# Performance work log

Hardware: AMD Instinct MI355X
Metric: run time of the kernel (lower is better)

## Reference

```python
import jax, jax.numpy as jnp
import numpy as np

NUM_QUBITS = 12
BOND_DIM = 8
DIM = 2 ** NUM_QUBITS  # 4096


def setup_inputs() -> dict:
    key = jax.random.key(0)
    k0, k1, k2, k3 = jax.random.split(key, 4)
    core0 = jax.random.normal(k0, (2, BOND_DIM), dtype=jnp.float32) * 0.5
    cores_mid = jax.random.normal(k1, (NUM_QUBITS - 2, BOND_DIM, 2, BOND_DIM), dtype=jnp.float32) * 0.5
    core_last = jax.random.normal(k2, (BOND_DIM, 2), dtype=jnp.float32) * 0.5
    A = jax.random.normal(k3, (DIM, DIM), dtype=jnp.float32)
    H = 0.5 * (A + A.T)  # Hamiltonians are symmetric
    return {"core0": core0, "cores_mid": cores_mid, "core_last": core_last, "H": H}


def _build_state(core0, cores_mid, core_last):
    # Sequential MPS contraction: state grows (2^k, D) site by site.
    state = core0  # (2, D)
    n_mid = cores_mid.shape[0]
    D = core0.shape[1]
    for i in range(n_mid):  # fixed, small layer loop (not a data-dim loop)
        # (S, a) x (a, p, b) -> (S, p, b) -> (S*2, b)
        state = jnp.einsum('sa,apb->spb', state, cores_mid[i]).reshape(-1, D)
    # (S, a) x (a, p) -> flat state vector of length 2^n
    psi = jnp.einsum('sa,ap->sp', state, core_last).reshape(-1)
    return psi


def reference(core0, cores_mid, core_last, H):
    psi = _build_state(core0, cores_mid, core_last)  # (2^n,)
    norm = jnp.dot(psi, psi)
    hpsi = H @ psi
    energy = jnp.dot(psi, hpsi) / norm          # <psi|H|psi>/<psi|psi>
    e2 = jnp.dot(psi, H @ hpsi) / norm          # <psi|H^2|psi>/<psi|psi>
    variance = jnp.maximum(e2 - energy * energy, 0.0)
    return jnp.stack([energy, variance])
```

## Files before the change

kernel.cpp:

```cpp
#include <hip/hip_runtime.h>
#include <hip/hip_bf16.h>


#define DIM 4096
#define BOND 8
#define NMID 10


__global__ __launch_bounds__(256) void build_psi_kernel(
    const float* __restrict__ core0,
    const float* __restrict__ cores_mid,
    const float* __restrict__ core_last,
    float* __restrict__ psi_g,
    double* __restrict__ acc) {
  __shared__ float c0[16];
  __shared__ float cm[NMID * 128];
  __shared__ float cl[16];

  if (threadIdx.x < 16) {
    c0[threadIdx.x] = core0[threadIdx.x];
    cl[threadIdx.x] = core_last[threadIdx.x];
  }
  for (int j = threadIdx.x; j < NMID * 128; j += 256) cm[j] = cores_mid[j];
  __syncthreads();

  const int idx = blockIdx.x * 256 + threadIdx.x;

  float v[BOND], nv[BOND];
  const int s0 = (idx >> 11) & 1;
#pragma unroll
  for (int a = 0; a < BOND; a++) v[a] = c0[s0 * BOND + a];

#pragma unroll
  for (int i = 0; i < NMID; i++) {
    const int p = (idx >> (10 - i)) & 1;
    const float* M = &cm[i * 128 + p * BOND];
#pragma unroll
    for (int b = 0; b < BOND; b++) nv[b] = v[0] * M[b];
#pragma unroll
    for (int a = 1; a < BOND; a++) {
#pragma unroll
      for (int b = 0; b < BOND; b++) nv[b] += v[a] * M[a * 16 + b];
    }
#pragma unroll
    for (int a = 0; a < BOND; a++) v[a] = nv[a];
  }

  const int pl = idx & 1;
  float ps = 0.f;
#pragma unroll
  for (int a = 0; a < BOND; a++) ps += v[a] * cl[a * 2 + pl];

  psi_g[idx] = ps;

  float sq = ps * ps;
#pragma unroll
  for (int off = 32; off > 0; off >>= 1) sq += __shfl_down(sq, off, 64);
  if ((threadIdx.x & 63) == 0) atomicAdd(&acc[0], (double)sq);
}

__global__ __launch_bounds__(256) void matvec_dots_kernel(
    const float* __restrict__ H,
    const float* __restrict__ psi_g,
    double* __restrict__ acc) {
  __shared__ float psi_s[DIM];
  __shared__ float wave_hpsi[4];

#pragma unroll
  for (int k = 0; k < 4; k++) {
    const int j = (k * 256 + threadIdx.x) * 4;
    *reinterpret_cast<float4*>(&psi_s[j]) =
        *reinterpret_cast<const float4*>(&psi_g[j]);
  }
  __syncthreads();

  const int wave = threadIdx.x >> 6;
  const int lane = threadIdx.x & 63;
  const int row = blockIdx.x * 4 + wave;
  const float* __restrict__ Hrow = H + (size_t)row * DIM;

  float sum = 0.f;
#pragma unroll
  for (int it = 0; it < 16; it++) {
    const int j = (it * 64 + lane) * 4;
    const float4 h = *reinterpret_cast<const float4*>(&Hrow[j]);
    const float4 p = *reinterpret_cast<const float4*>(&psi_s[j]);
    sum += h.x * p.x + h.y * p.y + h.z * p.z + h.w * p.w;
  }
#pragma unroll
  for (int off = 32; off > 0; off >>= 1) sum += __shfl_down(sum, off, 64);
  if (lane == 0) wave_hpsi[wave] = sum;
  __syncthreads();

  if (threadIdx.x == 0) {
    double ph = 0.0, hh = 0.0;
#pragma unroll
    for (int w = 0; w < 4; w++) {
      const double hp = (double)wave_hpsi[w];
      const double pr = (double)psi_s[blockIdx.x * 4 + w];
      ph += pr * hp;
      hh += hp * hp;
    }
    atomicAdd(&acc[1], ph);
    atomicAdd(&acc[2], hh);
  }
}

__global__ void finalize_kernel(const double* __restrict__ acc,
                                float* __restrict__ out) {
  const double norm = acc[0];
  const double e = acc[1] / norm;
  const double e2 = acc[2] / norm;
  double var = e2 - e * e;
  if (var < 0.0) var = 0.0;
  out[0] = (float)e;
  out[1] = (float)var;
}

extern "C" void kernel_launch(void* const* d_in, const int* in_sizes, int n_in,
                              void* d_out, int out_size, void* d_ws, size_t ws_size,
                              hipStream_t stream) {
  const float* core0 = (const float*)d_in[0];
  const float* cores_mid = (const float*)d_in[1];
  const float* core_last = (const float*)d_in[2];
  const float* H = (const float*)d_in[3];

  float* psi = (float*)d_ws;
  double* acc = (double*)((char*)d_ws + DIM * sizeof(float));

  hipMemsetAsync(acc, 0, 3 * sizeof(double), stream);
  build_psi_kernel<<<DIM / 256, 256, 0, stream>>>(core0, cores_mid, core_last, psi, acc);
  matvec_dots_kernel<<<DIM / 4, 256, 0, stream>>>(H, psi, acc);
  finalize_kernel<<<1, 1, 0, stream>>>(acc, (float*)d_out);
}
```

Baseline: 128.6 us.

## Exploit symmetry of H to read only upper-triangle tiles in matvec

Replaces the full row-wise matvec with a tiled symmetric matvec: each block handles one upper-triangular 128x128 tile of H and adds contributions to both y_I (via H x_J) and y_J (via H^T x_I). This roughly halves the HBM traffic for the 64 MB H read. Results go to hpsi through float atomics, and a single-block kernel then computes the norm, energy and variance, which removes the memset and finalize launches. In exchange it adds per-row wave shuffle reductions, float atomic contention on hpsi, and a serial loop in each block to decode its tile index.

After: 123.4 us. 4.0% less time.

```diff
diff --git a/kernel.cpp b/kernel.cpp
--- a/kernel.cpp
+++ b/kernel.cpp
@@ -5,6 +5,9 @@
 #define DIM 4096
 #define BOND 8
 #define NMID 10
+#define T 128
+#define NT (DIM / T)
+#define NPAIRS (NT * (NT + 1) / 2)
 
 
 __global__ __launch_bounds__(256) void build_psi_kernel(
@@ -12,7 +15,7 @@
     const float* __restrict__ cores_mid,
     const float* __restrict__ core_last,
     float* __restrict__ psi_g,
-    double* __restrict__ acc) {
+    float* __restrict__ hpsi_g) {
   __shared__ float c0[16];
   __shared__ float cm[NMID * 128];
   __shared__ float cl[16];
@@ -25,6 +28,7 @@
   __syncthreads();
 
   const int idx = blockIdx.x * 256 + threadIdx.x;
+  hpsi_g[idx] = 0.f;
 
   float v[BOND], nv[BOND];
   const int s0 = (idx >> 11) & 1;
@@ -52,69 +56,94 @@
   for (int a = 0; a < BOND; a++) ps += v[a] * cl[a * 2 + pl];
 
   psi_g[idx] = ps;
-
-  float sq = ps * ps;
-#pragma unroll
-  for (int off = 32; off > 0; off >>= 1) sq += __shfl_down(sq, off, 64);
-  if ((threadIdx.x & 63) == 0) atomicAdd(&acc[0], (double)sq);
 }
 
-__global__ __launch_bounds__(256) void matvec_dots_kernel(
+__global__ __launch_bounds__(256) void symv_kernel(
     const float* __restrict__ H,
     const float* __restrict__ psi_g,
-    double* __restrict__ acc) {
-  __shared__ float psi_s[DIM];
-  __shared__ float wave_hpsi[4];
+    float* __restrict__ hpsi_g) {
+  int rem = blockIdx.x;
+  int bi = 0;
+  while (rem >= NT - bi) { rem -= (NT - bi); ++bi; }
+  const int bj = bi + rem;
+  const bool diag = (bi == bj);
 
-#pragma unroll
-  for (int k = 0; k < 4; k++) {
-    const int j = (k * 256 + threadIdx.x) * 4;
-    *reinterpret_cast<float4*>(&psi_s[j]) =
-        *reinterpret_cast<const float4*>(&psi_g[j]);
+  __shared__ float xI[T], xJ[T], yI_s[T], yJp[4 * T];
+
+  if (threadIdx.x < T) {
+    xI[threadIdx.x] = psi_g[bi * T + threadIdx.x];
+    xJ[threadIdx.x] = psi_g[bj * T + threadIdx.x];
   }
   __syncthreads();
 
   const int wave = threadIdx.x >> 6;
   const int lane = threadIdx.x & 63;
-  const int row = blockIdx.x * 4 + wave;
-  const float* __restrict__ Hrow = H + (size_t)row * DIM;
+  const float* __restrict__ base = H + (size_t)(bi * T) * DIM + bj * T;
 
-  float sum = 0.f;
+  float aJx = 0.f, aJy = 0.f;
+  const float pJx = xJ[lane * 2], pJy = xJ[lane * 2 + 1];
+
+#pragma unroll 4
+  for (int k = 0; k < T / 4; ++k) {
+    const int r = k * 4 + wave;
+    const float2 a = *reinterpret_cast<const float2*>(base + (size_t)r * DIM + lane * 2);
+    const float xr = xI[r];
+    aJx += a.x * xr;
+    aJy += a.y * xr;
+    float d = a.x * pJx + a.y * pJy;
 #pragma unroll
-  for (int it = 0; it < 16; it++) {
-    const int j = (it * 64 + lane) * 4;
-    const float4 h = *reinterpret_cast<const float4*>(&Hrow[j]);
-    const float4 p = *reinterpret_cast<const float4*>(&psi_s[j]);
-    sum += h.x * p.x + h.y * p.y + h.z * p.z + h.w * p.w;
+    for (int off = 32; off > 0; off >>= 1) d += __shfl_down(d, off, 64);
+    if (lane == 0) yI_s[r] = d;
   }
-#pragma unroll
-  for (int off = 32; off > 0; off >>= 1) sum += __shfl_down(sum, off, 64);
-  if (lane == 0) wave_hpsi[wave] = sum;
+
+  yJp[wave * T + lane * 2] = aJx;
+  yJp[wave * T + lane * 2 + 1] = aJy;
   __syncthreads();
 
-  if (threadIdx.x == 0) {
-    double ph = 0.0, hh = 0.0;
-#pragma unroll
-    for (int w = 0; w < 4; w++) {
-      const double hp = (double)wave_hpsi[w];
-      const double pr = (double)psi_s[blockIdx.x * 4 + w];
-      ph += pr * hp;
-      hh += hp * hp;
+  if (threadIdx.x < T) {
+    atomicAdd(&hpsi_g[bi * T + threadIdx.x], yI_s[threadIdx.x]);
+    if (!diag) {
+      const float yj = yJp[threadIdx.x] + yJp[T + threadIdx.x] +
+                       yJp[2 * T + threadIdx.x] + yJp[3 * T + threadIdx.x];
+      atomicAdd(&hpsi_g[bj * T + threadIdx.x], yj);
     }
-    atomicAdd(&acc[1], ph);
-    atomicAdd(&acc[2], hh);
   }
 }
 
-__global__ void finalize_kernel(const double* __restrict__ acc,
-                                float* __restrict__ out) {
-  const double norm = acc[0];
-  const double e = acc[1] / norm;
-  const double e2 = acc[2] / norm;
-  double var = e2 - e * e;
-  if (var < 0.0) var = 0.0;
-  out[0] = (float)e;
-  out[1] = (float)var;
+__global__ __launch_bounds__(256) void dots_kernel(
+    const float* __restrict__ psi_g,
+    const float* __restrict__ hpsi_g,
+    float* __restrict__ out) {
+  __shared__ double s_n[4], s_ph[4], s_hh[4];
+  double n = 0.0, ph = 0.0, hh = 0.0;
+  for (int i = threadIdx.x; i < DIM; i += 256) {
+    const double p = (double)psi_g[i];
+    const double h = (double)hpsi_g[i];
+    n += p * p;
+    ph += p * h;
+    hh += h * h;
+  }
+#pragma unroll
+  for (int off = 32; off > 0; off >>= 1) {
+    n += __shfl_down(n, off, 64);
+    ph += __shfl_down(ph, off, 64);
+    hh += __shfl_down(hh, off, 64);
+  }
+  const int wave = threadIdx.x >> 6;
+  const int lane = threadIdx.x & 63;
+  if (lane == 0) { s_n[wave] = n; s_ph[wave] = ph; s_hh[wave] = hh; }
+  __syncthreads();
+  if (threadIdx.x == 0) {
+    double N = 0.0, P = 0.0, HH = 0.0;
+#pragma unroll
+    for (int w = 0; w < 4; w++) { N += s_n[w]; P += s_ph[w]; HH += s_hh[w]; }
+    const double e = P / N;
+    const double e2 = HH / N;
+    double var = e2 - e * e;
+    if (var < 0.0) var = 0.0;
+    out[0] = (float)e;
+    out[1] = (float)var;
+  }
 }
 
 extern "C" void kernel_launch(void* const* d_in, const int* in_sizes, int n_in,
@@ -126,10 +155,9 @@
   const float* H = (const float*)d_in[3];
 
   float* psi = (float*)d_ws;
-  double* acc = (double*)((char*)d_ws + DIM * sizeof(float));
+  float* hpsi = psi + DIM;
 
-  hipMemsetAsync(acc, 0, 3 * sizeof(double), stream);
-  build_psi_kernel<<<DIM / 256, 256, 0, stream>>>(core0, cores_mid, core_last, psi, acc);
-  matvec_dots_kernel<<<DIM / 4, 256, 0, stream>>>(H, psi, acc);
-  finalize_kernel<<<1, 1, 0, stream>>>(acc, (float*)d_out);
+  build_psi_kernel<<<DIM / 256, 256, 0, stream>>>(core0, cores_mid, core_last, psi, hpsi);
+  symv_kernel<<<NPAIRS, 256, 0, stream>>>(H, psi, hpsi);
+  dots_kernel<<<1, 256, 0, stream>>>(psi, hpsi, (float*)d_out);
 }
```
